# Optimization experiments

Measured on AMD Instinct MI355X. Metric: run time of the kernel, lower is better.

## Reference

```python
import jax, jax.numpy as jnp
import numpy as np

D_MODEL = 1024
NUM_HEADS = 16
HEAD_DIM = D_MODEL // NUM_HEADS
ROPE_BASE = 10000.0


def setup_inputs() -> dict:
    key = jax.random.key(0)
    ks = jax.random.split(key, 9)
    B, S = 2, 2048
    x = jax.random.normal(ks[0], (B, S, D_MODEL), dtype=jnp.float32)
    s = 1.0 / np.sqrt(D_MODEL)
    Wq = jax.random.normal(ks[1], (D_MODEL, D_MODEL), dtype=jnp.float32) * s
    bq = jnp.zeros((D_MODEL,), dtype=jnp.float32)
    Wk = jax.random.normal(ks[2], (D_MODEL, D_MODEL), dtype=jnp.float32) * s
    bk = jnp.zeros((D_MODEL,), dtype=jnp.float32)
    Wv = jax.random.normal(ks[3], (D_MODEL, D_MODEL), dtype=jnp.float32) * s
    bv = jnp.zeros((D_MODEL,), dtype=jnp.float32)
    Wo = jax.random.normal(ks[4], (D_MODEL, D_MODEL), dtype=jnp.float32) * s
    bo = jnp.zeros((D_MODEL,), dtype=jnp.float32)
    return {"x": x, "Wq": Wq, "bq": bq, "Wk": Wk, "bk": bk,
            "Wv": Wv, "bv": bv, "Wo": Wo, "bo": bo}


def _apply_rope(x):
    # x: [B, H, S, Dh]; interleaved complex-pair RoPE (torch.view_as_complex style)
    B, H, S, Dh = x.shape
    inv_freq = 1.0 / (ROPE_BASE ** (jnp.arange(0, Dh, 2, dtype=jnp.float32) / Dh))
    pos = jnp.arange(S, dtype=jnp.float32)
    freqs = pos[:, None] * inv_freq[None, :]            # [S, Dh/2]
    cos, sin = jnp.cos(freqs), jnp.sin(freqs)           # each [S, Dh/2]
    x2 = x.reshape(B, H, S, Dh // 2, 2)
    xr, xi = x2[..., 0], x2[..., 1]
    out_r = xr * cos - xi * sin
    out_i = xr * sin + xi * cos
    return jnp.stack([out_r, out_i], axis=-1).reshape(B, H, S, Dh)


def reference(x, Wq, bq, Wk, bk, Wv, bv, Wo, bo):
    B, S, _ = x.shape
    H, Dh = NUM_HEADS, HEAD_DIM
    def proj(W, b):
        y = jnp.einsum('bsd,ed->bse', x, W) + b          # torch Linear: x @ W.T + b
        return y.reshape(B, S, H, Dh).transpose(0, 2, 1, 3)  # [B,H,S,Dh]
    Q = _apply_rope(proj(Wq, bq))
    K = _apply_rope(proj(Wk, bk))
    V = proj(Wv, bv)
    scale = 1.0 / jnp.sqrt(jnp.float32(Dh))
    scores = jnp.einsum('bhqd,bhkd->bhqk', Q, K) * scale
    causal = jnp.tril(jnp.ones((S, S), dtype=bool))
    scores = jnp.where(causal, scores, jnp.float32(-jnp.inf))
    attn = jax.nn.softmax(scores, axis=-1)
    out = jnp.einsum('bhqk,bhkd->bhqd', attn, V)         # [B,H,S,Dh]
    out = out.transpose(0, 2, 1, 3).reshape(B, S, H * Dh)
    return jnp.einsum('bsd,ed->bse', out, Wo) + bo
```

## Files before the change

kernel.cpp:

```cpp
#include <hip/hip_runtime.h>
#include <stdint.h>

#define S_LEN 2048
#define BATCH 2
#define DM 1024
#define NH 16
#define DH 64
#define MROWS 4096

typedef unsigned short u16;
typedef unsigned int u32;
typedef __attribute__((ext_vector_type(8))) short bf16x8;
typedef __attribute__((ext_vector_type(4))) float f32x4;
typedef __attribute__((ext_vector_type(2))) unsigned u32x2;

union pack8 { u32 w[4]; bf16x8 v8; };

__device__ inline u16 f2bf(float f) {
  union { float f; unsigned u; } v; v.f = f;
  unsigned u = v.u;
  unsigned r = u + 0x7fffu + ((u >> 16) & 1u);
  return (u16)(r >> 16);
}

__device__ inline u32 pkbf(float lo, float hi) {
  u32 r;
  asm("v_cvt_pk_bf16_f32 %0, %1, %2" : "=v"(r) : "v"(lo), "v"(hi));
  return r;
}

__device__ inline float bf2f(short s) {
  union { u32 u; float f; } c; c.u = ((u32)(u16)s) << 16;
  return c.f;
}

__device__ __forceinline__ void gload_lds16(const u16* g, u16* l) {
  __builtin_amdgcn_global_load_lds(
      (const __attribute__((address_space(1))) u32*)g,
      (__attribute__((address_space(3))) u32*)l, 16, 0, 0);
}

__global__ void convert_k(const float* __restrict__ x, const float* __restrict__ wq,
                          const float* __restrict__ wk, const float* __restrict__ wv,
                          const float* __restrict__ wo, u16* __restrict__ xb,
                          u16* __restrict__ wb) {
  int i = blockIdx.x * blockDim.x + threadIdx.x;
  const int total = (MROWS * DM + 4 * DM * DM) / 4;
  if (i >= total) return;
  int e = i * 4;
  const float* src;
  u16* dst;
  if (e < MROWS * DM) {
    src = x + e; dst = xb + e;
  } else {
    int j = e - MROWS * DM;
    int w = j >> 20;
    int o = j & ((1 << 20) - 1);
    src = (w == 0) ? wq + o : (w == 1) ? wk + o : (w == 2) ? wv + o : wo + o;
    dst = wb + j;
  }
  float4 v = *(const float4*)src;
  uint2 r;
  r.x = (unsigned)f2bf(v.x) | ((unsigned)f2bf(v.y) << 16);
  r.y = (unsigned)f2bf(v.z) | ((unsigned)f2bf(v.w) << 16);
  *(uint2*)dst = r;
}

__global__ void rope_k(float2* __restrict__ tab, float* __restrict__ kmax) {
  int i = blockIdx.x * blockDim.x + threadIdx.x;
  if (i < 32) kmax[i] = 0.f;
  if (i >= S_LEN * 32) return;
  int s = i >> 5, p = i & 31;
  float inv = expf(-(float)p * 0.28782313662425575f);
  float a = (float)s * inv;
  tab[i] = make_float2(cosf(a), sinf(a));
}

__global__ void knorm_k(const u16* __restrict__ K, float* __restrict__ kmax) {
  const int row = blockIdx.x * 256 + threadIdx.x;
  const int bh = row >> 11;
  const u16* p = K + (size_t)row * DH;
  float ss = 0.f;
#pragma unroll
  for (int i = 0; i < 8; i++) {
    bf16x8 v = *(const bf16x8*)(p + i * 8);
#pragma unroll
    for (int j = 0; j < 8; j++) { float f = bf2f(v[j]); ss += f * f; }
  }
  float kn = sqrtf(ss);
#pragma unroll
  for (int d = 1; d < 64; d <<= 1) kn = fmaxf(kn, __shfl_xor(kn, d));
  if ((threadIdx.x & 63) == 0)
    atomicMax((unsigned*)(kmax + bh), __float_as_uint(kn));
}

__launch_bounds__(256)
__global__ void gemm_k(const u16* __restrict__ A,
                       const u16* __restrict__ w0, const u16* __restrict__ w1,
                       const u16* __restrict__ w2,
                       const float* __restrict__ b0, const float* __restrict__ b1,
                       const float* __restrict__ b2,
                       const float2* __restrict__ rope,
                       void* __restrict__ o0, void* __restrict__ o1, void* __restrict__ o2,
                       int mode0) {
  const int mode = mode0 + (int)(blockIdx.x >> 8);
  const int tile = blockIdx.x & 255;
  const int mt = tile >> 3, nt = tile & 7;
  const int mbase = mt * 128, nbase = nt * 128;
  const u16* W = (mode == 1) ? w1 : (mode == 2) ? w2 : w0;
  const float* bias = (mode == 1) ? b1 : (mode == 2) ? b2 : b0;
  void* outp = (mode == 1) ? o1 : (mode == 2) ? o2 : o0;

  __shared__ u16 As[128 * 32];
  __shared__ u16 Bs[128 * 32];

  const int t = threadIdx.x;
  const int lane = t & 63, wvi = t >> 6;
  const int lr = lane & 15, lg = lane >> 4;
  const int wm = (wvi >> 1) * 64, wn = (wvi & 1) * 64;

  f32x4 acc[4][4] = {};
  const int srow = t >> 2;
  const int scol = (t & 3) * 8;

  for (int kk = 0; kk < DM; kk += 32) {
    gload_lds16(A + (size_t)(mbase + srow) * DM + kk + scol, &As[wvi * 512]);
    gload_lds16(A + (size_t)(mbase + 64 + srow) * DM + kk + scol, &As[2048 + wvi * 512]);
    gload_lds16(W + (size_t)(nbase + srow) * DM + kk + scol, &Bs[wvi * 512]);
    gload_lds16(W + (size_t)(nbase + 64 + srow) * DM + kk + scol, &Bs[2048 + wvi * 512]);
    __syncthreads();

    bf16x8 af[4], bfr[4];
#pragma unroll
    for (int mi = 0; mi < 4; mi++)
      af[mi] = *(const bf16x8*)&As[(wm + mi * 16 + lr) * 32 + lg * 8];
#pragma unroll
    for (int ni = 0; ni < 4; ni++)
      bfr[ni] = *(const bf16x8*)&Bs[(wn + ni * 16 + lr) * 32 + lg * 8];
#pragma unroll
    for (int mi = 0; mi < 4; mi++)
#pragma unroll
      for (int ni = 0; ni < 4; ni++)
        acc[mi][ni] = __builtin_amdgcn_mfma_f32_16x16x32_bf16(af[mi], bfr[ni], acc[mi][ni], 0, 0, 0);
    __syncthreads();
  }

#pragma unroll
  for (int ni = 0; ni < 4; ni++) {
    const int col = nbase + wn + ni * 16 + lr;
    const float bv = bias[col];
#pragma unroll
    for (int mi = 0; mi < 4; mi++) {
      const int row0 = mbase + wm + mi * 16 + lg * 4;
      f32x4 v = acc[mi][ni];
#pragma unroll
      for (int r = 0; r < 4; r++) {
        float val = v[r] + bv;
        const int row = row0 + r;
        if (mode <= 1) {
          float nb = __shfl_xor(val, 1);
          const int d = col & 63, p = d >> 1, s = row & (S_LEN - 1);
          float2 cs = rope[s * 32 + p];
          float ov = (d & 1) ? (nb * cs.y + val * cs.x) : (val * cs.x - nb * cs.y);
          if (mode == 0) ov *= 0.18033688011112042f;
          const int b = row >> 11, h = col >> 6;
          ((u16*)outp)[((size_t)(b * NH + h) * S_LEN + s) * DH + d] = f2bf(ov);
        } else if (mode == 2) {
          const int b = row >> 11, h = col >> 6, d = col & 63, s = row & (S_LEN - 1);
          const int j = s & 31;
          const int pos = (s & ~31) + (((j & 15) >> 2) << 3) + ((j >> 4) << 2) + (j & 3);
          ((u16*)outp)[((size_t)(b * NH + h) * DH + d) * S_LEN + pos] = f2bf(val);
        } else {
          ((float*)outp)[(size_t)row * DM + col] = val;
        }
      }
    }
  }
}

__device__ __forceinline__ void sm_pv(const float a[8], float m, float& l,
                                      bf16x8 v0, bf16x8 v1, bf16x8 v2, bf16x8 v3,
                                      f32x4* o) {
  float p[8];
#pragma unroll
  for (int r = 0; r < 8; r++) p[r] = __builtin_amdgcn_exp2f(a[r] - m);
  l += ((p[0] + p[1]) + (p[2] + p[3])) + ((p[4] + p[5]) + (p[6] + p[7]));
  pack8 pu;
  pu.w[0] = pkbf(p[0], p[1]);
  pu.w[1] = pkbf(p[2], p[3]);
  pu.w[2] = pkbf(p[4], p[5]);
  pu.w[3] = pkbf(p[6], p[7]);
  o[0] = __builtin_amdgcn_mfma_f32_16x16x32_bf16(v0, pu.v8, o[0], 0, 0, 0);
  o[1] = __builtin_amdgcn_mfma_f32_16x16x32_bf16(v1, pu.v8, o[1], 0, 0, 0);
  o[2] = __builtin_amdgcn_mfma_f32_16x16x32_bf16(v2, pu.v8, o[2], 0, 0, 0);
  o[3] = __builtin_amdgcn_mfma_f32_16x16x32_bf16(v3, pu.v8, o[3], 0, 0, 0);
}

__launch_bounds__(64)
__global__ void attn_k(const u16* __restrict__ Q, const u16* __restrict__ K,
                       const u16* __restrict__ Vt, u16* __restrict__ Oo,
                       const float* __restrict__ kmax) {
  const int bh = blockIdx.x & 31;
  const int tile = (int)(blockIdx.x >> 5);
  const int qbase = tile * 32;
  const int nst = tile + 1;
  const int lane = threadIdx.x;
  const int lr = lane & 15, lg = lane >> 4;

  __shared__ u16 Ks[2][2048];
  __shared__ u16 Vs[2][2048];

  const u16* Kg = K + (size_t)bh * S_LEN * DH;
  const u16* Vg = Vt + (size_t)bh * DH * S_LEN;

  const int krow = lane >> 3;
  const int ksoff = ((((lane & 7) << 4) ^ ((lane >> 3) << 4)) >> 1);
  const int vrow = lane >> 2;
  const int vsoff = ((((lane & 3) << 4) ^ (((lane >> 3) & 3) << 4)) >> 1);

  const size_t qoff = ((size_t)bh * S_LEN + qbase + lr) * DH + lg * 8;
  const bf16x8 qA0 = *(const bf16x8*)(Q + qoff);
  const bf16x8 qA1 = *(const bf16x8*)(Q + qoff + 32);
  const bf16x8 qB0 = *(const bf16x8*)(Q + qoff + 16 * DH);
  const bf16x8 qB1 = *(const bf16x8*)(Q + qoff + 16 * DH + 32);

  float ssA = 0.f, ssB = 0.f;
#pragma unroll
  for (int j = 0; j < 8; j++) {
    float a0 = bf2f(qA0[j]), a1 = bf2f(qA1[j]);
    float b0 = bf2f(qB0[j]), b1 = bf2f(qB1[j]);
    ssA += a0 * a0 + a1 * a1;
    ssB += b0 * b0 + b1 * b1;
  }
  ssA += __shfl_xor(ssA, 16); ssA += __shfl_xor(ssA, 32);
  ssB += __shfl_xor(ssB, 16); ssB += __shfl_xor(ssB, 32);
  const float kmx = kmax[bh];
  const float mA = sqrtf(ssA) * kmx;
  const float mB = sqrtf(ssB) * kmx;

  f32x4 oA[4] = {}, oB[4] = {};
  float lA = 0.f, lB = 0.f;
  const f32x4 zero = {};

  const int kmsk = (lr & 7) << 4;
  const int k00 = lr * 64 + (((lg << 4)) ^ kmsk) / 2;
  const int k01 = lr * 64 + ((64 + (lg << 4)) ^ kmsk) / 2;
  const int k10 = (16 + lr) * 64 + (((lg << 4)) ^ kmsk) / 2;
  const int k11 = (16 + lr) * 64 + ((64 + (lg << 4)) ^ kmsk) / 2;
  const int vmsk = ((lr >> 1) & 3) << 4;
  const int vo = ((lg << 4) ^ vmsk) / 2;

#define STAGE(s32, bb)                                                          \
  {                                                                             \
    const u16* kgs = Kg + (size_t)(s32) * DH;                                   \
    const u16* vgs = Vg + (s32);                                                \
    _Pragma("unroll")                                                           \
    for (int i = 0; i < 4; i++)                                                 \
      gload_lds16(kgs + (size_t)(i * 8 + krow) * DH + ksoff, &Ks[bb][i * 512]); \
    _Pragma("unroll")                                                           \
    for (int i = 0; i < 4; i++)                                                 \
      gload_lds16(vgs + (size_t)(i * 16 + vrow) * S_LEN + vsoff, &Vs[bb][i * 512]); \
  }

  STAGE(0, 0);

  for (int s = 0; s < nst; ++s) {
    const int b = s & 1;
    if (s + 1 < nst) {
      STAGE((s + 1) * 32, b ^ 1);
      asm volatile("s_waitcnt vmcnt(8)" ::: "memory");
    } else {
      asm volatile("s_waitcnt vmcnt(0)" ::: "memory");
    }

    const u16* Kb = Ks[b];
    const u16* Vb = Vs[b];
    bf16x8 kc0 = *(const bf16x8*)&Kb[k00];
    bf16x8 kc1 = *(const bf16x8*)&Kb[k01];
    bf16x8 kc2 = *(const bf16x8*)&Kb[k10];
    bf16x8 kc3 = *(const bf16x8*)&Kb[k11];
    bf16x8 v0 = *(const bf16x8*)&Vb[(lr) * 32 + vo];
    bf16x8 v1 = *(const bf16x8*)&Vb[(16 + lr) * 32 + vo];
    bf16x8 v2 = *(const bf16x8*)&Vb[(32 + lr) * 32 + vo];
    bf16x8 v3 = *(const bf16x8*)&Vb[(48 + lr) * 32 + vo];

    f32x4 s0A = __builtin_amdgcn_mfma_f32_16x16x32_bf16(kc0, qA0, zero, 0, 0, 0);
    s0A = __builtin_amdgcn_mfma_f32_16x16x32_bf16(kc1, qA1, s0A, 0, 0, 0);
    f32x4 s1A = __builtin_amdgcn_mfma_f32_16x16x32_bf16(kc2, qA0, zero, 0, 0, 0);
    s1A = __builtin_amdgcn_mfma_f32_16x16x32_bf16(kc3, qA1, s1A, 0, 0, 0);
    f32x4 s0B = __builtin_amdgcn_mfma_f32_16x16x32_bf16(kc0, qB0, zero, 0, 0, 0);
    s0B = __builtin_amdgcn_mfma_f32_16x16x32_bf16(kc1, qB1, s0B, 0, 0, 0);
    f32x4 s1B = __builtin_amdgcn_mfma_f32_16x16x32_bf16(kc2, qB0, zero, 0, 0, 0);
    s1B = __builtin_amdgcn_mfma_f32_16x16x32_bf16(kc3, qB1, s1B, 0, 0, 0);

    const int qrelA = qbase + lr - (s << 5) - (lg << 2);
    const int qrelB = qrelA + 16;
    float aA[8], aB[8];
#pragma unroll
    for (int r = 0; r < 4; r++) {
      aA[r]     = (r <= qrelA)      ? s0A[r] : -__builtin_inff();
      aA[4 + r] = (r + 16 <= qrelA) ? s1A[r] : -__builtin_inff();
      aB[r]     = (r <= qrelB)      ? s0B[r] : -__builtin_inff();
      aB[4 + r] = (r + 16 <= qrelB) ? s1B[r] : -__builtin_inff();
    }
    sm_pv(aA, mA, lA, v0, v1, v2, v3, oA);
    sm_pv(aB, mB, lB, v0, v1, v2, v3, oB);
  }
#undef STAGE

  lA += __shfl_xor(lA, 16); lA += __shfl_xor(lA, 32);
  lB += __shfl_xor(lB, 16); lB += __shfl_xor(lB, 32);
  const float rlA = __builtin_amdgcn_rcpf(lA);
  const float rlB = __builtin_amdgcn_rcpf(lB);

  const int bb = bh >> 4, h = bh & 15;
  const size_t obaseA = ((size_t)bb * S_LEN + qbase + lr) * DM + h * DH;
  const size_t obaseB = obaseA + (size_t)16 * DM;
#pragma unroll
  for (int dt = 0; dt < 4; dt++) {
    u32x2 pkA, pkB;
    pkA.x = pkbf(oA[dt][0] * rlA, oA[dt][1] * rlA);
    pkA.y = pkbf(oA[dt][2] * rlA, oA[dt][3] * rlA);
    pkB.x = pkbf(oB[dt][0] * rlB, oB[dt][1] * rlB);
    pkB.y = pkbf(oB[dt][2] * rlB, oB[dt][3] * rlB);
    *(u32x2*)(Oo + obaseA + dt * 16 + lg * 4) = pkA;
    *(u32x2*)(Oo + obaseB + dt * 16 + lg * 4) = pkB;
  }
}

extern "C" void kernel_launch(void* const* d_in, const int* in_sizes, int n_in,
                              void* d_out, int out_size, void* d_ws, size_t ws_size,
                              hipStream_t stream) {
  const float* x  = (const float*)d_in[0];
  const float* Wq = (const float*)d_in[1];
  const float* bq = (const float*)d_in[2];
  const float* Wk = (const float*)d_in[3];
  const float* bk = (const float*)d_in[4];
  const float* Wv = (const float*)d_in[5];
  const float* bv = (const float*)d_in[6];
  const float* Wo = (const float*)d_in[7];
  const float* bo = (const float*)d_in[8];

  char* ws = (char*)d_ws;
  u16* xb    = (u16*)(ws);
  u16* wb    = (u16*)(ws + (8u << 20));
  u16* Qb    = (u16*)(ws + (16u << 20));
  u16* Kb    = (u16*)(ws + (24u << 20));
  u16* Vtb   = (u16*)(ws + (32u << 20));
  u16* AOb   = (u16*)(ws + (40u << 20));
  float2* rt = (float2*)(ws + (48u << 20));
  float* kmx = (float*)(ws + (48u << 20) + (512u << 10));

  convert_k<<<8192, 256, 0, stream>>>(x, Wq, Wk, Wv, Wo, xb, wb);
  rope_k<<<256, 256, 0, stream>>>(rt, kmx);
  gemm_k<<<768, 256, 0, stream>>>(xb, wb, wb + (1u << 20), wb + (2u << 20),
                                  bq, bk, bv, rt, Qb, Kb, Vtb, 0);
  knorm_k<<<256, 256, 0, stream>>>(Kb, kmx);
  attn_k<<<2048, 64, 0, stream>>>(Qb, Kb, Vtb, AOb, kmx);
  gemm_k<<<256, 256, 0, stream>>>(AOb, wb + (3u << 20), wb + (3u << 20), wb + (3u << 20),
                                  bo, bo, bo, rt, d_out, d_out, d_out, 3);
}
```

Measured before the change: 150.7 us.

## Split long causal attention tiles across two blocks and combine partials

Query tiles 32-63 of the causal attention kernel are each split into two blocks that cover halves of the key range. Each half writes an unnormalised bf16 partial output and its row sums into reused workspace, and a new reduce kernel adds the halves and normalises. This is meant to cut the tail caused by the longest blocks, which process up to 64 key tiles. The cost is an extra kernel launch, extra global traffic for the partials, and some bf16 rounding of the partial outputs.

```diff
diff --git a/kernel.cpp b/kernel.cpp
--- a/kernel.cpp
+++ b/kernel.cpp
@@ -199,11 +199,21 @@
 __launch_bounds__(64)
 __global__ void attn_k(const u16* __restrict__ Q, const u16* __restrict__ K,
                        const u16* __restrict__ Vt, u16* __restrict__ Oo,
-                       const float* __restrict__ kmax) {
-  const int bh = blockIdx.x & 31;
-  const int tile = (int)(blockIdx.x >> 5);
+                       const float* __restrict__ kmax,
+                       u16* __restrict__ po, float* __restrict__ pl) {
+  int bh, tile, s0, s1, pidx = 0, split;
+  if (blockIdx.x < 1024) {
+    bh = blockIdx.x & 31; tile = (int)(blockIdx.x >> 5);
+    s0 = 0; s1 = tile + 1; split = 0;
+  } else {
+    const int idx = (int)blockIdx.x - 1024;
+    bh = idx & 31; tile = 32 + ((idx >> 5) & 31);
+    const int half = idx >> 10;
+    const int nst = tile + 1, h = nst >> 1;
+    s0 = half ? h : 0; s1 = half ? nst : h;
+    pidx = idx; split = 1;
+  }
   const int qbase = tile * 32;
-  const int nst = tile + 1;
   const int lane = threadIdx.x;
   const int lr = lane & 15, lg = lane >> 4;
 
@@ -262,11 +272,11 @@
       gload_lds16(vgs + (size_t)(i * 16 + vrow) * S_LEN + vsoff, &Vs[bb][i * 512]); \
   }
 
-  STAGE(0, 0);
-
-  for (int s = 0; s < nst; ++s) {
+  STAGE(s0 * 32, s0 & 1);
+
+  for (int s = s0; s < s1; ++s) {
     const int b = s & 1;
-    if (s + 1 < nst) {
+    if (s + 1 < s1) {
       STAGE((s + 1) * 32, b ^ 1);
       asm volatile("s_waitcnt vmcnt(8)" ::: "memory");
     } else {
@@ -310,22 +320,62 @@
 
   lA += __shfl_xor(lA, 16); lA += __shfl_xor(lA, 32);
   lB += __shfl_xor(lB, 16); lB += __shfl_xor(lB, 32);
-  const float rlA = __builtin_amdgcn_rcpf(lA);
-  const float rlB = __builtin_amdgcn_rcpf(lB);
-
-  const int bb = bh >> 4, h = bh & 15;
-  const size_t obaseA = ((size_t)bb * S_LEN + qbase + lr) * DM + h * DH;
-  const size_t obaseB = obaseA + (size_t)16 * DM;
-#pragma unroll
-  for (int dt = 0; dt < 4; dt++) {
-    u32x2 pkA, pkB;
-    pkA.x = pkbf(oA[dt][0] * rlA, oA[dt][1] * rlA);
-    pkA.y = pkbf(oA[dt][2] * rlA, oA[dt][3] * rlA);
-    pkB.x = pkbf(oB[dt][0] * rlB, oB[dt][1] * rlB);
-    pkB.y = pkbf(oB[dt][2] * rlB, oB[dt][3] * rlB);
-    *(u32x2*)(Oo + obaseA + dt * 16 + lg * 4) = pkA;
-    *(u32x2*)(Oo + obaseB + dt * 16 + lg * 4) = pkB;
-  }
+
+  if (!split) {
+    const float rlA = __builtin_amdgcn_rcpf(lA);
+    const float rlB = __builtin_amdgcn_rcpf(lB);
+    const int bb = bh >> 4, h = bh & 15;
+    const size_t obaseA = ((size_t)bb * S_LEN + qbase + lr) * DM + h * DH;
+    const size_t obaseB = obaseA + (size_t)16 * DM;
+#pragma unroll
+    for (int dt = 0; dt < 4; dt++) {
+      u32x2 pkA, pkB;
+      pkA.x = pkbf(oA[dt][0] * rlA, oA[dt][1] * rlA);
+      pkA.y = pkbf(oA[dt][2] * rlA, oA[dt][3] * rlA);
+      pkB.x = pkbf(oB[dt][0] * rlB, oB[dt][1] * rlB);
+      pkB.y = pkbf(oB[dt][2] * rlB, oB[dt][3] * rlB);
+      *(u32x2*)(Oo + obaseA + dt * 16 + lg * 4) = pkA;
+      *(u32x2*)(Oo + obaseB + dt * 16 + lg * 4) = pkB;
+    }
+  } else {
+    u16* pb = po + (size_t)pidx * 2048;
+#pragma unroll
+    for (int dt = 0; dt < 4; dt++) {
+      const int dbase = dt * 16 + lg * 4;
+      u32x2 pkA, pkB;
+      pkA.x = pkbf(oA[dt][0], oA[dt][1]);
+      pkA.y = pkbf(oA[dt][2], oA[dt][3]);
+      pkB.x = pkbf(oB[dt][0], oB[dt][1]);
+      pkB.y = pkbf(oB[dt][2], oB[dt][3]);
+      *(u32x2*)(pb + lr * 64 + dbase) = pkA;
+      *(u32x2*)(pb + (16 + lr) * 64 + dbase) = pkB;
+    }
+    if (lg == 0) {
+      pl[pidx * 32 + lr] = lA;
+      pl[pidx * 32 + 16 + lr] = lB;
+    }
+  }
+}
+
+__global__ void reduce_k(const u16* __restrict__ po, const float* __restrict__ pl,
+                         u16* __restrict__ Oo) {
+  const int i = blockIdx.x * 256 + threadIdx.x;
+  const int dg = i & 7;
+  const int q = (i >> 3) & 31;
+  const int tt = (i >> 8) & 31;
+  const int bh = i >> 13;
+  const int p0 = tt * 32 + bh, p1 = 1024 + p0;
+  const bf16x8 a = *(const bf16x8*)(po + (size_t)p0 * 2048 + q * 64 + dg * 8);
+  const bf16x8 b = *(const bf16x8*)(po + (size_t)p1 * 2048 + q * 64 + dg * 8);
+  const float rl = __builtin_amdgcn_rcpf(pl[p0 * 32 + q] + pl[p1 * 32 + q]);
+  pack8 r;
+#pragma unroll
+  for (int j = 0; j < 4; j++)
+    r.w[j] = pkbf((bf2f(a[2 * j]) + bf2f(b[2 * j])) * rl,
+                  (bf2f(a[2 * j + 1]) + bf2f(b[2 * j + 1])) * rl);
+  const int s = (32 + tt) * 32 + q;
+  u16* dst = Oo + ((size_t)(bh >> 4) * S_LEN + s) * DM + (bh & 15) * DH + dg * 8;
+  *(bf16x8*)dst = r.v8;
 }
 
 extern "C" void kernel_launch(void* const* d_in, const int* in_sizes, int n_in,
@@ -351,12 +401,16 @@
   float2* rt = (float2*)(ws + (48u << 20));
   float* kmx = (float*)(ws + (48u << 20) + (512u << 10));
 
+  u16* po   = xb;
+  float* pl = (float*)rt;
+
   convert_k<<<8192, 256, 0, stream>>>(x, Wq, Wk, Wv, Wo, xb, wb);
   rope_k<<<256, 256, 0, stream>>>(rt, kmx);
   gemm_k<<<768, 256, 0, stream>>>(xb, wb, wb + (1u << 20), wb + (2u << 20),
                                   bq, bk, bv, rt, Qb, Kb, Vtb, 0);
   knorm_k<<<256, 256, 0, stream>>>(Kb, kmx);
-  attn_k<<<2048, 64, 0, stream>>>(Qb, Kb, Vtb, AOb, kmx);
+  attn_k<<<3072, 64, 0, stream>>>(Qb, Kb, Vtb, AOb, kmx, po, pl);
+  reduce_k<<<1024, 256, 0, stream>>>(po, pl, AOb);
   gemm_k<<<256, 256, 0, stream>>>(AOb, wb + (3u << 20), wb + (3u << 20), wb + (3u << 20),
                                   bo, bo, bo, rt, d_out, d_out, d_out, 3);
 }
```

After: 149.7 us. About the same (-0.7%).
